# Kernel optimization log

Hardware: AMD Instinct MI355X
Metric: run time of the kernel (lower is better)

## Reference

```python
import jax, jax.numpy as jnp
import numpy as np
from jax.scipy.special import digamma

EPS = 2.2e-10      # real_min in WHAI_Decoder
MBRATIO = 100.0    # args.MBratio
EPSIT = 1.0        # epsit[0] after normalization, MBObserved == 0

V = 30000
KS = [128, 64, 32]
B = 512


def _col_norm_phi(k, shape):
    p = 0.2 + 0.8 * jax.random.uniform(k, shape, dtype=jnp.float32)
    return p / jnp.maximum(EPS, p.sum(0))


def setup_inputs() -> dict:
    key = jax.random.key(0)
    ks = jax.random.split(key, 10)
    inp = {
        'x': jax.random.uniform(ks[0], (B, V), dtype=jnp.float32) * 5.0,  # nonneg count-like data
        'theta0': jax.random.uniform(ks[1], (KS[0], B), dtype=jnp.float32) + 0.1,
        'theta1': jax.random.uniform(ks[2], (KS[1], B), dtype=jnp.float32) + 0.1,
        'theta2': jax.random.uniform(ks[3], (KS[2], B), dtype=jnp.float32) + 0.1,
        'phi0': _col_norm_phi(ks[4], (V, KS[0])),
        'phi1': _col_norm_phi(ks[5], (KS[0], KS[1])),
        'phi2': _col_norm_phi(ks[6], (KS[1], KS[2])),
        'noise0': jax.random.normal(ks[7], (V, KS[0]), dtype=jnp.float32),
        'noise1': jax.random.normal(ks[8], (KS[0], KS[1]), dtype=jnp.float32),
        'noise2': jax.random.normal(ks[9], (KS[1], KS[2]), dtype=jnp.float32),
    }
    return inp


def _update_phi(x, thetas, phis, noises):
    # x: (B, V); thetas[t]: (K_t, B); phis[0]: (V, K0), phis[t]: (K_{t-1}, K_t)
    x_cur = x.T  # (V, B) counts flowing up the hierarchy
    new_phis = []
    for t in range(len(phis)):
        phi, theta = phis[t], thetas[t]
        denom = jnp.maximum(phi @ theta, EPS)                 # (D_t, B)
        if t == 0:
            # expected multinomial augmentation (multi_aug)
            ratio = x_cur / denom                             # (V, B)
        else:
            # expected CRT counts (crt_multi_aug): E[m] = p*(psi(p+x)-psi(p))
            m = denom * (digamma(denom + x_cur) - digamma(denom))
            ratio = m / denom                                 # (K_{t-1}, B)
        WSZS = phi * (ratio @ theta.T)                        # (D_t, K_t)
        x_cur = theta * (phi.T @ ratio)                       # Xt_to_t1: (K_t, B)
        # TLASGR-MCMC step (MBObserved == 0 branch)
        EWSZS = MBRATIO * WSZS
        NDot = EWSZS.sum(0)                                   # (K_t,)
        inv_n = 1.0 / jnp.maximum(NDot, EPS)
        tmp = EWSZS + 0.1
        step = phi + EPSIT * inv_n * (tmp - tmp.sum(0) * phi) \
               + jnp.sqrt(EPSIT * 2.0 * inv_n * phi) * noises[t]
        # ProjSimplexSpecial
        p = step - (step.sum(0) - 1.0) * phi
        p = jnp.maximum(EPS, p)
        new_phis.append(p / jnp.maximum(EPS, p.sum(0)))
    return new_phis


def reference(x, theta0, theta1, theta2, phi0, phi1, phi2, noise0, noise1, noise2):
    new_phis = _update_phi(x, [theta0, theta1, theta2], [phi0, phi1, phi2],
                           [noise0, noise1, noise2])
    return jnp.concatenate([p.ravel() for p in new_phis])
```

## Files before the change

### kernel.cpp

```cpp
#include <hip/hip_runtime.h>
#include <math.h>

#define EPSF 2.2e-10f
#define NV 30000
#define NVP 30080
#define NB 512

typedef __attribute__((ext_vector_type(8))) short short8;
typedef __attribute__((ext_vector_type(4))) float f32x4;
typedef __attribute__((ext_vector_type(4))) unsigned short ushort4v;

__device__ __forceinline__ unsigned short f2bf(float f) {
    unsigned int u = __float_as_uint(f);
    u += 0x7fffu + ((u >> 16) & 1u);
    return (unsigned short)(u >> 16);
}
__device__ __forceinline__ float bf2f(unsigned short h) {
    return __uint_as_float((unsigned int)h << 16);
}

__device__ __forceinline__ float digammaf(float xx) {
    float x = xx, r = 0.f;
    while (x < 6.f) { r -= 1.f / x; x += 1.f; }
    float f = 1.f / (x * x);
    float s = logf(x) - 0.5f / x
        - f * (0.0833333333f - f * (0.0083333333f - f * (0.0039682540f
        - f * (0.0041666667f - f * 0.0075757576f))));
    return r + s;
}

__global__ __launch_bounds__(256) void pk_theta(
    const float* __restrict__ th, unsigned short* __restrict__ th_bf,
    unsigned short* __restrict__ thT_bf)
{
    int idx = blockIdx.x * 256 + threadIdx.x;
    int k = idx >> 7, b4 = (idx & 127) << 2;
    float4 v = *(const float4*)&th[k * NB + b4];
    ushort4v h = { f2bf(v.x), f2bf(v.y), f2bf(v.z), f2bf(v.w) };
    *(ushort4v*)&th_bf[k * NB + b4] = h;
#pragma unroll
    for (int i = 0; i < 4; ++i) thT_bf[(b4 + i) * 128 + k] = h[i];
}

#define K1_PHI(v,k)    ((((v) << 8) + ((k) << 1)) ^ (((v) & 7) << 4))

__global__ __launch_bounds__(512, 8) void kA1(
    const float* __restrict__ phi0,
    const unsigned short* __restrict__ thT_bf,
    const float* __restrict__ noise0,
    unsigned short* __restrict__ denomT,
    unsigned short* __restrict__ phiT,
    float* __restrict__ Sphi,
    float* __restrict__ Snz)
{
    __shared__ __align__(16) unsigned char lds[18432];
    const int t = threadIdx.x, lane = t & 63, w = t >> 6;
    const int lrow = lane & 15, hi = lane >> 4;
    const int lkb = hi << 3, lcq = hi << 2;
    const int vbase = (blockIdx.x >> 2) << 6;
    const int bslice = blockIdx.x & 3;
    const int bb = (bslice << 7) + (w << 4);

    for (int idx = t; idx < 1024; idx += 512) {
        int v = idx >> 4, kc = (idx & 15) << 3;
        int vg = vbase + v;
        float4 a = {0,0,0,0}, b = {0,0,0,0};
        if (vg < NV) {
            a = *(const float4*)&phi0[(size_t)vg * 128 + kc];
            b = *(const float4*)&phi0[(size_t)vg * 128 + kc + 4];
        }
        ushort4v h0 = { f2bf(a.x), f2bf(a.y), f2bf(a.z), f2bf(a.w) };
        ushort4v h1 = { f2bf(b.x), f2bf(b.y), f2bf(b.z), f2bf(b.w) };
        *(ushort4v*)&lds[K1_PHI(v, kc)]     = h0;
        *(ushort4v*)&lds[K1_PHI(v, kc + 4)] = h1;
    }
    __syncthreads();

    if (bslice == 0) {
        for (int idx = t; idx < 8192; idx += 512) {
            int v = idx & 63, k = idx >> 6;
            phiT[(size_t)k * NVP + vbase + v] = *(const unsigned short*)&lds[K1_PHI(v, k)];
        }
    }

    f32x4 dacc[4];
#pragma unroll
    for (int vg = 0; vg < 4; ++vg) dacc[vg] = (f32x4){0.f, 0.f, 0.f, 0.f};
#pragma unroll
    for (int ks = 0; ks < 4; ++ks) {
        short8 bt = *(const short8*)&thT_bf[(size_t)(bb + lrow) * 128 + (ks << 5) + lkb];
#pragma unroll
        for (int vg = 0; vg < 4; ++vg) {
            short8 pa = *(const short8*)&lds[K1_PHI(vg * 16 + lrow, (ks << 5) + lkb)];
            dacc[vg] = __builtin_amdgcn_mfma_f32_16x16x32_bf16(pa, bt, dacc[vg], 0, 0, 0);
        }
    }
#pragma unroll
    for (int vg = 0; vg < 4; ++vg) {
        ushort4v h;
#pragma unroll
        for (int i = 0; i < 4; ++i) h[i] = f2bf(dacc[vg][i]);
        *(ushort4v*)&denomT[(size_t)(bb + lrow) * NVP + vbase + vg * 16 + lcq] = h;
    }

    if (bslice == 0) {
        const int kf = t & 127, vh = t >> 7;
        float sp = 0.f, sn = 0.f;
#pragma unroll
        for (int vi = 0; vi < 16; ++vi) {
            int v = (vh << 4) + vi;
            int vg = vbase + v;
            if (vg < NV) {
                float ph = bf2f(*(const unsigned short*)&lds[K1_PHI(v, kf)]);
                sp += ph;
                sn += sqrtf(ph) * noise0[(size_t)vg * 128 + kf];
            }
        }
        float* red = (float*)&lds[16384];
        red[t] = sp;
        __syncthreads();
        if (t < 128) atomicAdd(&Sphi[t], (red[t] + red[t + 128]) + (red[t + 256] + red[t + 384]));
        __syncthreads();
        red[t] = sn;
        __syncthreads();
        if (t < 128) atomicAdd(&Snz[t], (red[t] + red[t + 128]) + (red[t + 256] + red[t + 384]));
    }
}

__global__ __launch_bounds__(256, 8) void kA2(
    const float* __restrict__ x,
    unsigned short* __restrict__ ratioT)
{
    const int b = blockIdx.x >> 2;
    const int q = blockIdx.x & 3;
    const float* xr = x + (size_t)b * NV;
    unsigned short* rr = ratioT + (size_t)b * NVP;
    const int base = q * 7500;
#pragma unroll
    for (int i = 0; i < 8; ++i) {
        int vi = i * 256 + threadIdx.x;
        if (vi < 1875) {
            int v = base + vi * 4;
            f32x4 xv = *(const f32x4*)&xr[v];
            ushort4v dh = *(const ushort4v*)&rr[v];
            ushort4v h;
#pragma unroll
            for (int j = 0; j < 4; ++j) {
                float den = fmaxf(bf2f(dh[j]), EPSF);
                h[j] = f2bf(xv[j] * __builtin_amdgcn_rcpf(den));
            }
            *(ushort4v*)&rr[v] = h;
        }
    }
}

#define KB_RT(v,b) ((((v) << 7) + ((b) << 1)) ^ (((((v) & 7) ^ (((v) >> 3) & 7))) << 4))
#define KB_R0(v,k) ((((v) << 9) + ((k) << 2)) ^ (((v) & 7) << 4))
#define K2_PH(k,v) ((((k) << 7) + ((v) << 1)) ^ (((k) & 7) << 4))
#define K2_RT(b,v) ((16384 + ((b) << 7) + ((v) << 1)) ^ (((b) & 7) << 4))

__global__ __launch_bounds__(512, 4) void kBC(
    const unsigned short* __restrict__ ratioT,
    const unsigned short* __restrict__ th_bf,
    const unsigned short* __restrict__ phiT,
    const float* __restrict__ phi0,
    float* __restrict__ R0,
    float* __restrict__ NDot0,
    float* __restrict__ part)
{
    __shared__ __align__(16) unsigned char lds[32768];
    const int t = threadIdx.x, lane = t & 63, w = t >> 6;
    const int lrow = lane & 15, hi = lane >> 4;
    const int lkb = hi << 3, lcq = hi << 2;

    if (blockIdx.x < 470) {
        const int vbase = blockIdx.x << 6;
        f32x4 racc[4];
#pragma unroll
        for (int vf = 0; vf < 4; ++vf) racc[vf] = (f32x4){0.f, 0.f, 0.f, 0.f};

        for (int c = 0; c < 8; ++c) {
            const int bs = c << 6;
            __syncthreads();
            {
                int b = t >> 3, v8 = (t & 7) << 3;
                short8 val = *(const short8*)&ratioT[(size_t)(bs + b) * NVP + vbase + v8];
#pragma unroll
                for (int j = 0; j < 8; ++j)
                    *(unsigned short*)&lds[KB_RT(v8 + j, b)] = ((unsigned short*)&val)[j];
            }
            __syncthreads();
#pragma unroll
            for (int ks = 0; ks < 2; ++ks) {
                short8 a0 = *(const short8*)&th_bf[(size_t)(w * 16 + lrow) * NB + bs + (ks << 5) + lkb];
#pragma unroll
                for (int vf = 0; vf < 4; ++vf) {
                    short8 bb = *(const short8*)&lds[KB_RT(vf * 16 + lrow, (ks << 5) + lkb)];
                    racc[vf] = __builtin_amdgcn_mfma_f32_16x16x32_bf16(a0, bb, racc[vf], 0, 0, 0);
                }
            }
        }
        __syncthreads();
#pragma unroll
        for (int vf = 0; vf < 4; ++vf)
            *(f32x4*)&lds[KB_R0(vf * 16 + lrow, w * 16 + lcq)] = racc[vf];
        __syncthreads();
        const int kf = t & 127;
        float nd = 0.f;
        for (int idx = t; idx < 8192; idx += 512) {
            int v = idx >> 7;
            int vg = vbase + v;
            if (vg < NV) {
                float r0v = *(const float*)&lds[KB_R0(v, kf)];
                R0[(size_t)vg * 128 + kf] = r0v;
                nd += r0v * phi0[(size_t)vg * 128 + kf];
            }
        }
        __syncthreads();
        float* red = (float*)lds;
        red[t] = nd;
        __syncthreads();
        if (t < 128) atomicAdd(&NDot0[t], 100.f * ((red[t] + red[t + 128]) + (red[t + 256] + red[t + 384])));
    } else {
        const int bid2 = blockIdx.x - 470;
        const int btile = bid2 & 7;
        const int split = bid2 >> 3;
        const int b0 = btile << 6;

        f32x4 acc[4];
#pragma unroll
        for (int bt = 0; bt < 4; ++bt) acc[bt] = (f32x4){0.f, 0.f, 0.f, 0.f};

        for (int ci = split; ci < 470; ci += 80) {
            const int v0 = ci << 6;
            __syncthreads();
            for (int idx = t; idx < 1024; idx += 512) {
                int k = idx >> 3, v8 = (idx & 7) << 3;
                *(short8*)&lds[K2_PH(k, v8)] =
                    *(const short8*)&phiT[(size_t)k * NVP + v0 + v8];
            }
            {
                int b = t >> 3, v8 = (t & 7) << 3;
                *(short8*)&lds[K2_RT(b, v8)] =
                    *(const short8*)&ratioT[(size_t)(b0 + b) * NVP + v0 + v8];
            }
            __syncthreads();
#pragma unroll
            for (int vs = 0; vs < 2; ++vs) {
                short8 a0 = *(const short8*)&lds[K2_PH(w * 16 + lrow, (vs << 5) + lkb)];
#pragma unroll
                for (int bt = 0; bt < 4; ++bt) {
                    short8 bb = *(const short8*)&lds[K2_RT(bt * 16 + lrow, (vs << 5) + lkb)];
                    acc[bt] = __builtin_amdgcn_mfma_f32_16x16x32_bf16(a0, bb, acc[bt], 0, 0, 0);
                }
            }
        }
        float* dst = part + (size_t)split * 65536;
#pragma unroll
        for (int bt = 0; bt < 4; ++bt)
#pragma unroll
            for (int i = 0; i < 4; ++i)
                dst[(w * 16 + lcq + i) * NB + b0 + bt * 16 + lrow] = acc[bt][i];
    }
}

__global__ __launch_bounds__(256) void k3456(
    const float* __restrict__ phi0, const float* __restrict__ noise0,
    const float* __restrict__ NDot0, const float* __restrict__ Sphi,
    const float* __restrict__ Snz, float* __restrict__ out,
    const float* __restrict__ phi1, const float* __restrict__ theta1,
    const float* __restrict__ theta0, const float* __restrict__ part,
    float* __restrict__ ratio1)
{
    const int t = threadIdx.x;
    if (blockIdx.x < 1875) {
        const int k = t & 127;
        const size_t base = (size_t)blockIdx.x * 2048;
        float ndv = NDot0[k];
        float inv_n = 1.f / fmaxf(ndv, EPSF);
        float tmpsum = ndv + 3000.f;
        float sp = Sphi[k], sn = Snz[k];
        float stepsum = sp + inv_n * tmpsum * (1.f - sp) + sqrtf(2.f * inv_n) * sn;
        float ssm1 = stepsum - 1.f;
        float psum = stepsum - ssm1 * sp;
        float inv = 1.f / fmaxf(psum, EPSF);
#pragma unroll
        for (int i = 0; i < 8; ++i) {
            size_t e = base + i * 256 + t;
            float phi = phi0[e], R = out[e], nz = noise0[e];
            float tmp = fmaf(100.f * phi, R, 0.1f);
            float step = phi + inv_n * (tmp - tmpsum * phi) + sqrtf(2.f * inv_n * phi) * nz;
            float p = fmaxf(EPSF, step - ssm1 * phi);
            out[e] = p * inv;
        }
    } else {
        int g = (blockIdx.x - 1875) * 256 + t;
        int d = g >> 9, b = g & 511;
        float c0a = 0.f, c0b = 0.f, c0c = 0.f, c0d = 0.f;
        for (int s = 0; s < 80; s += 4) {
            c0a += part[(size_t)s * 65536 + g];
            c0b += part[(size_t)(s + 1) * 65536 + g];
            c0c += part[(size_t)(s + 2) * 65536 + g];
            c0d += part[(size_t)(s + 3) * 65536 + g];
        }
        float c0 = (c0a + c0b) + (c0c + c0d);
        float denom = 0.f;
        for (int k = 0; k < 64; ++k) denom = fmaf(phi1[d * 64 + k], theta1[k * NB + b], denom);
        denom = fmaxf(denom, EPSF);
        float xc = theta0[g] * c0;
        ratio1[g] = digammaf(denom + xc) - digammaf(denom);
    }
}

__global__ __launch_bounds__(256) void k78(
    const float* __restrict__ ratio1, const float* __restrict__ theta1,
    const float* __restrict__ phi1, float* __restrict__ R1,
    float* __restrict__ ndp1, float* __restrict__ x2v)
{
    if (blockIdx.x < 256) {
        const int wid = (blockIdx.x << 2) + (threadIdx.x >> 6);
        const int lane = threadIdx.x & 63;
        const int kk = wid & 63, dg = wid >> 6;
        float th[8];
#pragma unroll
        for (int j = 0; j < 8; ++j) th[j] = theta1[kk * NB + j * 64 + lane];
        float ndp = 0.f;
#pragma unroll
        for (int dd = 0; dd < 8; ++dd) {
            int d = dg * 8 + dd;
            float s = 0.f;
#pragma unroll
            for (int j = 0; j < 8; ++j)
                s = fmaf(ratio1[d * NB + j * 64 + lane], th[j], s);
#pragma unroll
            for (int o = 1; o < 64; o <<= 1) s += __shfl_xor(s, o);
            if (lane == dd) {
                R1[d * 64 + kk] = s;
                ndp = phi1[d * 64 + kk] * s;
            }
        }
#pragma unroll
        for (int o = 1; o < 8; o <<= 1) ndp += __shfl_xor(ndp, o);
        if (lane == 0) ndp1[dg * 64 + kk] = 100.f * ndp;
    } else {
        int g = (blockIdx.x - 256) * 256 + threadIdx.x;
        int kk = g >> 9, b = g & 511;
        float s0 = 0.f, s1 = 0.f, s2 = 0.f, s3 = 0.f;
#pragma unroll 4
        for (int d = 0; d < 128; d += 4) {
            s0 = fmaf(phi1[d * 64 + kk],       ratio1[d * NB + b],       s0);
            s1 = fmaf(phi1[(d + 1) * 64 + kk], ratio1[(d + 1) * NB + b], s1);
            s2 = fmaf(phi1[(d + 2) * 64 + kk], ratio1[(d + 2) * NB + b], s2);
            s3 = fmaf(phi1[(d + 3) * 64 + kk], ratio1[(d + 3) * NB + b], s3);
        }
        x2v[g] = theta1[g] * ((s0 + s1) + (s2 + s3));
    }
}

__global__ __launch_bounds__(256) void k10t1(
    const float* __restrict__ phi2, const float* __restrict__ theta2,
    const float* __restrict__ x2v, float* __restrict__ ratio2,
    const float* __restrict__ phi1, const float* __restrict__ R1,
    const float* __restrict__ noise1, const float* __restrict__ ndp1,
    float* __restrict__ out1)
{
    __shared__ float red[8];
    if (blockIdx.x < 128) {
        int g = blockIdx.x * 256 + threadIdx.x;
        int d = g >> 9, b = g & 511;
        float denom = 0.f;
        for (int k = 0; k < 32; ++k) denom = fmaf(phi2[d * 32 + k], theta2[k * NB + b], denom);
        denom = fmaxf(denom, EPSF);
        float xc = x2v[g];
        ratio2[g] = digammaf(denom + xc) - digammaf(denom);
    } else {
        const int t = threadIdx.x;
        const int c = t >> 7;
        const int k = (blockIdx.x - 128) * 2 + c;
        const int d = t & 127;
        const int e = d * 64 + k;
        float ndv = 0.f;
#pragma unroll
        for (int i = 0; i < 16; ++i) ndv += ndp1[i * 64 + k];
        float inv_n = 1.f / fmaxf(ndv, EPSF);
        float tmpsum = ndv + 12.8f;
        float phiv = phi1[e];
        float tmp = fmaf(100.f * phiv, R1[e], 0.1f);
        float step = phiv + inv_n * (tmp - tmpsum * phiv) + sqrtf(2.f * inv_n * phiv) * noise1[e];
        float s = step;
#pragma unroll
        for (int o = 1; o < 64; o <<= 1) s += __shfl_xor(s, o);
        int slot = t >> 6;
        if ((t & 63) == 0) red[slot] = s;
        __syncthreads();
        float ssum = red[c * 2] + red[c * 2 + 1];
        float p = fmaxf(EPSF, step - (ssum - 1.f) * phiv);
        float q = p;
#pragma unroll
        for (int o = 1; o < 64; o <<= 1) q += __shfl_xor(q, o);
        if ((t & 63) == 0) red[4 + slot] = q;
        __syncthreads();
        float psum = red[4 + c * 2] + red[4 + c * 2 + 1];
        out1[e] = p / fmaxf(psum, EPSF);
    }
}

__global__ __launch_bounds__(256) void k11_r2_w(
    const float* __restrict__ ratio2, const float* __restrict__ theta2,
    const float* __restrict__ phi2, float* __restrict__ R2, float* __restrict__ ndp2)
{
    const int wid = (blockIdx.x << 2) + (threadIdx.x >> 6);
    const int lane = threadIdx.x & 63;
    const int kk = wid & 31, dg = wid >> 5;
    float th[8];
#pragma unroll
    for (int j = 0; j < 8; ++j) th[j] = theta2[kk * NB + j * 64 + lane];
    float ndp = 0.f;
#pragma unroll
    for (int dd = 0; dd < 8; ++dd) {
        int d = dg * 8 + dd;
        float s = 0.f;
#pragma unroll
        for (int j = 0; j < 8; ++j)
            s = fmaf(ratio2[d * NB + j * 64 + lane], th[j], s);
#pragma unroll
        for (int o = 1; o < 64; o <<= 1) s += __shfl_xor(s, o);
        if (lane == dd) {
            R2[d * 32 + kk] = s;
            ndp = phi2[d * 32 + kk] * s;
        }
    }
#pragma unroll
    for (int o = 1; o < 8; o <<= 1) ndp += __shfl_xor(ndp, o);
    if (lane == 0) ndp2[dg * 32 + kk] = 100.f * ndp;
}

__global__ __launch_bounds__(256) void t2_quad(
    const float* __restrict__ phi2, const float* __restrict__ R2,
    const float* __restrict__ noise2, const float* __restrict__ ndp2,
    float* __restrict__ out2)
{
    const int c = blockIdx.x * 4 + (threadIdx.x >> 6);
    const int d = threadIdx.x & 63;
    const int e = d * 32 + c;
    float ndv = 0.f;
#pragma unroll
    for (int i = 0; i < 8; ++i) ndv += ndp2[i * 32 + c];
    float inv_n = 1.f / fmaxf(ndv, EPSF);
    float tmpsum = ndv + 6.4f;
    float phiv = phi2[e];
    float tmp = fmaf(100.f * phiv, R2[e], 0.1f);
    float step = phiv + inv_n * (tmp - tmpsum * phiv) + sqrtf(2.f * inv_n * phiv) * noise2[e];
    float s = step;
#pragma unroll
    for (int o = 1; o < 64; o <<= 1) s += __shfl_xor(s, o);
    float p = fmaxf(EPSF, step - (s - 1.f) * phiv);
    float q = p;
#pragma unroll
    for (int o = 1; o < 64; o <<= 1) q += __shfl_xor(q, o);
    out2[e] = p / fmaxf(q, EPSF);
}

extern "C" void kernel_launch(void* const* d_in, const int* in_sizes, int n_in,
                              void* d_out, int out_size, void* d_ws, size_t ws_size,
                              hipStream_t stream)
{
    const float* x      = (const float*)d_in[0];
    const float* theta0 = (const float*)d_in[1];
    const float* theta1 = (const float*)d_in[2];
    const float* theta2 = (const float*)d_in[3];
    const float* phi0   = (const float*)d_in[4];
    const float* phi1   = (const float*)d_in[5];
    const float* phi2   = (const float*)d_in[6];
    const float* noise0 = (const float*)d_in[7];
    const float* noise1 = (const float*)d_in[8];
    const float* noise2 = (const float*)d_in[9];
    float* out = (float*)d_out;
    float* ws  = (float*)d_ws;

    unsigned short* ratioT = (unsigned short*)ws;
    unsigned short* phiT   = (unsigned short*)(ws + 7700480);
    unsigned short* thT_bf = (unsigned short*)(ws + 9625600);
    unsigned short* th_bf  = (unsigned short*)(ws + 9658368);
    float* part     = ws + 9691136;
    float* NDot0    = ws + 14934016;
    float* Sphi     = ws + 14934144;
    float* Snz      = ws + 14934272;
    float* ndp1     = ws + 14934400;
    float* ndp2     = ws + 14935424;
    float* ratio1   = ws + 14935680;
    float* R1       = ws + 15001216;
    float* x2v      = ws + 15009408;
    float* ratio2   = ws + 15042176;
    float* R2       = ws + 15074944;

    (void)hipMemsetAsync(NDot0, 0, 384 * sizeof(float), stream);

    pk_theta<<<64, 256, 0, stream>>>(theta0, th_bf, thT_bf);

    kA1<<<1880, 512, 0, stream>>>(phi0, thT_bf, noise0, ratioT, phiT, Sphi, Snz);
    kA2<<<2048, 256, 0, stream>>>(x, ratioT);
    kBC<<<1110, 512, 0, stream>>>(ratioT, th_bf, phiT, phi0, out, NDot0, part);
    k3456<<<2131, 256, 0, stream>>>(phi0, noise0, NDot0, Sphi, Snz, out,
                                    phi1, theta1, theta0, part, ratio1);

    k78<<<384, 256, 0, stream>>>(ratio1, theta1, phi1, R1, ndp1, x2v);
    k10t1<<<160, 256, 0, stream>>>(phi2, theta2, x2v, ratio2,
                                   phi1, R1, noise1, ndp1, out + 3840000);

    k11_r2_w<<<64, 256, 0, stream>>>(ratio2, theta2, phi2, R2, ndp2);
    t2_quad<<<8, 256, 0, stream>>>(phi2, R2, noise2, ndp2, out + 3848192);
}
```

Measured before the change: 139.8 us.

## Split phi0 preprocessing into dedicated kernel and enlarge kA1 tiles

Adds a kPre kernel that converts phi0 to bf16 once (row-major and transposed), computes the Sphi/Snz column sums as per-block partials, and absorbs the theta bf16 packing. kA1 then loads bf16 phi directly, covers 128 vocabulary rows per block with 8 MFMA accumulators, and no longer does transpose or reduction work only in its bslice==0 blocks. The atomics are replaced by a deterministic partial reduction done in an extra kA2 block, and the LDS swizzle changes. In exchange it adds an extra pass writing and re-reading phi_bf through global memory, reuses the part buffer for it, and doubles kA1's LDS and register use.

Result: slower. 152.7 us (+9.2%).

```diff
diff --git a/kernel.cpp b/kernel.cpp
--- a/kernel.cpp
+++ b/kernel.cpp
@@ -29,108 +29,151 @@
     return r + s;
 }
 
-__global__ __launch_bounds__(256) void pk_theta(
-    const float* __restrict__ th, unsigned short* __restrict__ th_bf,
-    unsigned short* __restrict__ thT_bf)
-{
-    int idx = blockIdx.x * 256 + threadIdx.x;
-    int k = idx >> 7, b4 = (idx & 127) << 2;
-    float4 v = *(const float4*)&th[k * NB + b4];
-    ushort4v h = { f2bf(v.x), f2bf(v.y), f2bf(v.z), f2bf(v.w) };
-    *(ushort4v*)&th_bf[k * NB + b4] = h;
-#pragma unroll
-    for (int i = 0; i < 4; ++i) thT_bf[(b4 + i) * 128 + k] = h[i];
-}
-
-#define K1_PHI(v,k)    ((((v) << 8) + ((k) << 1)) ^ (((v) & 7) << 4))
+#define PRE(v,k) ((((v) << 8) + ((k) << 1)) ^ (((((v) & 7) ^ (((v) >> 3) & 7))) << 4))
+
+__global__ __launch_bounds__(512) void kPre(
+    const float* __restrict__ phi0,
+    const float* __restrict__ noise0,
+    const float* __restrict__ th,
+    unsigned short* __restrict__ phi_bf,
+    unsigned short* __restrict__ phiT,
+    unsigned short* __restrict__ th_bf,
+    unsigned short* __restrict__ thT_bf,
+    float* __restrict__ Sp_part,
+    float* __restrict__ Sn_part)
+{
+    const int t = threadIdx.x;
+    if (blockIdx.x >= 235) {
+        int idx = (blockIdx.x - 235) * 512 + t;
+        int k = idx >> 7, b4 = (idx & 127) << 2;
+        float4 v = *(const float4*)&th[k * NB + b4];
+        ushort4v h = { f2bf(v.x), f2bf(v.y), f2bf(v.z), f2bf(v.w) };
+        *(ushort4v*)&th_bf[k * NB + b4] = h;
+#pragma unroll
+        for (int i = 0; i < 4; ++i) thT_bf[(b4 + i) * 128 + k] = h[i];
+        return;
+    }
+    __shared__ __align__(16) unsigned char lds[34816];
+    const int vbase = blockIdx.x << 7;
+
+    for (int idx = t; idx < 2048; idx += 512) {
+        int v = idx >> 4, k0 = (idx & 15) << 3;
+        int vg = vbase + v;
+        float4 a = {0,0,0,0}, b = {0,0,0,0};
+        if (vg < NV) {
+            a = *(const float4*)&phi0[(size_t)vg * 128 + k0];
+            b = *(const float4*)&phi0[(size_t)vg * 128 + k0 + 4];
+        }
+        ushort4v h0 = { f2bf(a.x), f2bf(a.y), f2bf(a.z), f2bf(a.w) };
+        ushort4v h1 = { f2bf(b.x), f2bf(b.y), f2bf(b.z), f2bf(b.w) };
+        *(ushort4v*)&lds[PRE(v, k0)]     = h0;
+        *(ushort4v*)&lds[PRE(v, k0 + 4)] = h1;
+    }
+    __syncthreads();
+    for (int idx = t; idx < 2048; idx += 512) {
+        int v = idx >> 4, k0 = (idx & 15) << 3;
+        int vg = vbase + v;
+        if (vg < NV)
+            *(short8*)&phi_bf[(size_t)vg * 128 + k0] = *(const short8*)&lds[PRE(v, k0)];
+    }
+    for (int idx = t; idx < 2048; idx += 512) {
+        int k = idx >> 4, v8 = (idx & 15) << 3;
+        ushort4v ha, hb;
+#pragma unroll
+        for (int j = 0; j < 4; ++j) {
+            ha[j] = *(const unsigned short*)&lds[PRE(v8 + j, k)];
+            hb[j] = *(const unsigned short*)&lds[PRE(v8 + 4 + j, k)];
+        }
+        *(ushort4v*)&phiT[(size_t)k * NVP + vbase + v8]     = ha;
+        *(ushort4v*)&phiT[(size_t)k * NVP + vbase + v8 + 4] = hb;
+    }
+    const int kf = t & 127, vgr = t >> 7;
+    float sp = 0.f, sn = 0.f;
+#pragma unroll
+    for (int vi = 0; vi < 32; ++vi) {
+        int v = (vgr << 5) + vi;
+        int vg = vbase + v;
+        if (vg < NV) {
+            float ph = bf2f(*(const unsigned short*)&lds[PRE(v, kf)]);
+            sp += ph;
+            sn += sqrtf(ph) * noise0[(size_t)vg * 128 + kf];
+        }
+    }
+    float* red = (float*)&lds[32768];
+    red[t] = sp;
+    __syncthreads();
+    if (t < 128) Sp_part[blockIdx.x * 128 + t] =
+        (red[t] + red[t + 128]) + (red[t + 256] + red[t + 384]);
+    __syncthreads();
+    red[t] = sn;
+    __syncthreads();
+    if (t < 128) Sn_part[blockIdx.x * 128 + t] =
+        (red[t] + red[t + 128]) + (red[t + 256] + red[t + 384]);
+}
 
 __global__ __launch_bounds__(512, 8) void kA1(
-    const float* __restrict__ phi0,
+    const unsigned short* __restrict__ phi_bf,
     const unsigned short* __restrict__ thT_bf,
-    const float* __restrict__ noise0,
-    unsigned short* __restrict__ denomT,
-    unsigned short* __restrict__ phiT,
-    float* __restrict__ Sphi,
-    float* __restrict__ Snz)
-{
-    __shared__ __align__(16) unsigned char lds[18432];
+    unsigned short* __restrict__ denomT)
+{
+    __shared__ __align__(16) unsigned char lds[32768];
     const int t = threadIdx.x, lane = t & 63, w = t >> 6;
     const int lrow = lane & 15, hi = lane >> 4;
     const int lkb = hi << 3, lcq = hi << 2;
-    const int vbase = (blockIdx.x >> 2) << 6;
+    const int vbase = (blockIdx.x >> 2) << 7;
     const int bslice = blockIdx.x & 3;
     const int bb = (bslice << 7) + (w << 4);
 
-    for (int idx = t; idx < 1024; idx += 512) {
-        int v = idx >> 4, kc = (idx & 15) << 3;
+    for (int idx = t; idx < 2048; idx += 512) {
+        int v = idx >> 4, k0 = (idx & 15) << 3;
         int vg = vbase + v;
-        float4 a = {0,0,0,0}, b = {0,0,0,0};
-        if (vg < NV) {
-            a = *(const float4*)&phi0[(size_t)vg * 128 + kc];
-            b = *(const float4*)&phi0[(size_t)vg * 128 + kc + 4];
-        }
-        ushort4v h0 = { f2bf(a.x), f2bf(a.y), f2bf(a.z), f2bf(a.w) };
-        ushort4v h1 = { f2bf(b.x), f2bf(b.y), f2bf(b.z), f2bf(b.w) };
-        *(ushort4v*)&lds[K1_PHI(v, kc)]     = h0;
-        *(ushort4v*)&lds[K1_PHI(v, kc + 4)] = h1;
+        short8 val = {0,0,0,0,0,0,0,0};
+        if (vg < NV) val = *(const short8*)&phi_bf[(size_t)vg * 128 + k0];
+        *(short8*)&lds[PRE(v, k0)] = val;
     }
     __syncthreads();
 
-    if (bslice == 0) {
-        for (int idx = t; idx < 8192; idx += 512) {
-            int v = idx & 63, k = idx >> 6;
-            phiT[(size_t)k * NVP + vbase + v] = *(const unsigned short*)&lds[K1_PHI(v, k)];
-        }
-    }
-
-    f32x4 dacc[4];
-#pragma unroll
-    for (int vg = 0; vg < 4; ++vg) dacc[vg] = (f32x4){0.f, 0.f, 0.f, 0.f};
+    f32x4 dacc[8];
+#pragma unroll
+    for (int vg = 0; vg < 8; ++vg) dacc[vg] = (f32x4){0.f, 0.f, 0.f, 0.f};
 #pragma unroll
     for (int ks = 0; ks < 4; ++ks) {
         short8 bt = *(const short8*)&thT_bf[(size_t)(bb + lrow) * 128 + (ks << 5) + lkb];
 #pragma unroll
-        for (int vg = 0; vg < 4; ++vg) {
-            short8 pa = *(const short8*)&lds[K1_PHI(vg * 16 + lrow, (ks << 5) + lkb)];
+        for (int vg = 0; vg < 8; ++vg) {
+            short8 pa = *(const short8*)&lds[PRE(vg * 16 + lrow, (ks << 5) + lkb)];
             dacc[vg] = __builtin_amdgcn_mfma_f32_16x16x32_bf16(pa, bt, dacc[vg], 0, 0, 0);
         }
     }
 #pragma unroll
-    for (int vg = 0; vg < 4; ++vg) {
+    for (int vg = 0; vg < 8; ++vg) {
         ushort4v h;
 #pragma unroll
         for (int i = 0; i < 4; ++i) h[i] = f2bf(dacc[vg][i]);
         *(ushort4v*)&denomT[(size_t)(bb + lrow) * NVP + vbase + vg * 16 + lcq] = h;
     }
-
-    if (bslice == 0) {
-        const int kf = t & 127, vh = t >> 7;
-        float sp = 0.f, sn = 0.f;
-#pragma unroll
-        for (int vi = 0; vi < 16; ++vi) {
-            int v = (vh << 4) + vi;
-            int vg = vbase + v;
-            if (vg < NV) {
-                float ph = bf2f(*(const unsigned short*)&lds[K1_PHI(v, kf)]);
-                sp += ph;
-                sn += sqrtf(ph) * noise0[(size_t)vg * 128 + kf];
-            }
-        }
-        float* red = (float*)&lds[16384];
-        red[t] = sp;
-        __syncthreads();
-        if (t < 128) atomicAdd(&Sphi[t], (red[t] + red[t + 128]) + (red[t + 256] + red[t + 384]));
-        __syncthreads();
-        red[t] = sn;
-        __syncthreads();
-        if (t < 128) atomicAdd(&Snz[t], (red[t] + red[t + 128]) + (red[t + 256] + red[t + 384]));
-    }
 }
 
 __global__ __launch_bounds__(256, 8) void kA2(
     const float* __restrict__ x,
-    unsigned short* __restrict__ ratioT)
-{
+    unsigned short* __restrict__ ratioT,
+    const float* __restrict__ Sp_part, const float* __restrict__ Sn_part,
+    float* __restrict__ Sphi, float* __restrict__ Snz)
+{
+    if (blockIdx.x == 2048) {
+        const int t = threadIdx.x;
+        if (t < 128) {
+            float s = 0.f;
+            for (int i = 0; i < 235; ++i) s += Sp_part[i * 128 + t];
+            Sphi[t] = s;
+        } else {
+            const int k = t - 128;
+            float s = 0.f;
+            for (int i = 0; i < 235; ++i) s += Sn_part[i * 128 + k];
+            Snz[k] = s;
+        }
+        return;
+    }
     const int b = blockIdx.x >> 2;
     const int q = blockIdx.x & 3;
     const float* xr = x + (size_t)b * NV;
@@ -483,23 +526,27 @@
     unsigned short* thT_bf = (unsigned short*)(ws + 9625600);
     unsigned short* th_bf  = (unsigned short*)(ws + 9658368);
     float* part     = ws + 9691136;
+    unsigned short* phi_bf = (unsigned short*)part;
     float* NDot0    = ws + 14934016;
     float* Sphi     = ws + 14934144;
     float* Snz      = ws + 14934272;
     float* ndp1     = ws + 14934400;
     float* ndp2     = ws + 14935424;
-    float* ratio1   = ws + 14935680;
-    float* R1       = ws + 15001216;
-    float* x2v      = ws + 15009408;
-    float* ratio2   = ws + 15042176;
-    float* R2       = ws + 15074944;
-
-    (void)hipMemsetAsync(NDot0, 0, 384 * sizeof(float), stream);
-
-    pk_theta<<<64, 256, 0, stream>>>(theta0, th_bf, thT_bf);
-
-    kA1<<<1880, 512, 0, stream>>>(phi0, thT_bf, noise0, ratioT, phiT, Sphi, Snz);
-    kA2<<<2048, 256, 0, stream>>>(x, ratioT);
+    float* Sp_part  = ws + 14935680;
+    float* Sn_part  = ws + 14965760;
+    float* ratio1   = ws + 14995840;
+    float* R1       = ws + 15061376;
+    float* x2v      = ws + 15069568;
+    float* ratio2   = ws + 15102336;
+    float* R2       = ws + 15135104;
+
+    (void)hipMemsetAsync(NDot0, 0, 128 * sizeof(float), stream);
+
+    kPre<<<267, 512, 0, stream>>>(phi0, noise0, theta0, phi_bf, phiT,
+                                  th_bf, thT_bf, Sp_part, Sn_part);
+
+    kA1<<<940, 512, 0, stream>>>(phi_bf, thT_bf, ratioT);
+    kA2<<<2049, 256, 0, stream>>>(x, ratioT, Sp_part, Sn_part, Sphi, Snz);
     kBC<<<1110, 512, 0, stream>>>(ratioT, th_bf, phiT, phi0, out, NDot0, part);
     k3456<<<2131, 256, 0, stream>>>(phi0, noise0, NDot0, Sphi, Snz, out,
                                     phi1, theta1, theta0, part, ratio1);
```
